# Performance work log

Measured on AMD Instinct MI355X. Metric: run time of the kernel, lower is better.

The kernel has to match this reference:

```python
import jax, jax.numpy as jnp
import numpy as np

BATCH = 256
NUM_PIXELS = 4096
NUM_LATENT = 8192
NUM_STEPS = 50
STEP_SIZE = 0.1
SPARSE_MULT = 0.1
EPS = 1e-8


def setup_inputs() -> dict:
    key = jax.random.key(0)
    k1, k2 = jax.random.split(key)
    input_tensor = jax.random.normal(k1, (BATCH, NUM_PIXELS), dtype=jnp.float32)
    w = jax.random.normal(k2, (NUM_PIXELS, NUM_LATENT), dtype=jnp.float32)
    # l2-normalize each dictionary element (column over pixel dim), as in dp.l2_normalize_weights
    w = w / (jnp.linalg.norm(w, axis=0, keepdims=True) + EPS)
    return {"input_tensor": input_tensor, "w": w}


def _threshold(u):
    # soft threshold with rectify_a=True: a = max(u - lambda, 0)
    return jnp.where(u > SPARSE_MULT, u - SPARSE_MULT, jnp.zeros_like(u))


def reference(input_tensor, w):
    # excitatory drive b = x @ w, constant over inference steps  [B, L]
    excitatory = jnp.matmul(input_tensor, w)
    # inhibitory Gram matrix G = w^T w - I  [L, L]
    gram = jnp.matmul(w.T, w) - jnp.eye(NUM_LATENT, dtype=w.dtype)

    def body(u, _):
        a = _threshold(u)
        du = excitatory - jnp.matmul(a, gram) - u
        return u + STEP_SIZE * du, None

    u0 = jnp.zeros((input_tensor.shape[0], NUM_LATENT), dtype=input_tensor.dtype)
    u_final, _ = jax.lax.scan(body, u0, None, length=NUM_STEPS - 1)
    a_final = _threshold(u_final)
    # reconstruction = a @ w^T  [B, P]
    return jnp.matmul(a_final, w.T)
```

## Files before the change

kernel.cpp:

```cpp
#include <hip/hip_runtime.h>
#include <stdint.h>

#define B_DIM 256
#define P_DIM 4096
#define L_DIM 8192
#define NSTEPS 50
#define STEP 0.1f
#define LAM 0.1f
#define FP8_ITERS 40
#define GSCALE 64.0f
#define ASCALE 16.0f
#define INV_SCALE (1.0f / (64.0f * 16.0f))

typedef __attribute__((ext_vector_type(8))) short bf16x8;
typedef __attribute__((ext_vector_type(4))) float f32x4;
typedef __attribute__((ext_vector_type(2))) long lgx2;

__device__ __forceinline__ unsigned short f2bf(float f) {
    union { float f; uint32_t u; } x; x.f = f;
    uint32_t r = (x.u + 0x7FFF + ((x.u >> 16) & 1)) >> 16;
    return (unsigned short)r;
}
__device__ __forceinline__ float bf2f(unsigned short h) {
    union { uint32_t u; float f; } x; x.u = (uint32_t)h << 16; return x.f;
}


__global__ void cast_x_kernel(const float* __restrict__ in, unsigned short* __restrict__ out, int n) {
    int i = (blockIdx.x * blockDim.x + threadIdx.x) * 4;
    if (i < n) {
        float4 v = *(const float4*)&in[i];
        ushort4 o;
        o.x = f2bf(v.x); o.y = f2bf(v.y); o.z = f2bf(v.z); o.w = f2bf(v.w);
        *(ushort4*)&out[i] = o;
    }
}

__global__ void cast_transpose_w(const float* __restrict__ w,
                                 unsigned short* __restrict__ w_bf,
                                 unsigned short* __restrict__ wT_bf) {
    __shared__ float tile[32][33];
    int c0 = blockIdx.x * 32;
    int r0 = blockIdx.y * 32;
    int tx = threadIdx.x, ty = threadIdx.y;
#pragma unroll
    for (int i = ty; i < 32; i += 8) {
        float v = w[(size_t)(r0 + i) * L_DIM + c0 + tx];
        tile[i][tx] = v;
        w_bf[(size_t)(r0 + i) * L_DIM + c0 + tx] = f2bf(v);
    }
    __syncthreads();
#pragma unroll
    for (int i = ty; i < 32; i += 8) {
        wT_bf[(size_t)(c0 + i) * P_DIM + r0 + tx] = f2bf(tile[tx][i]);
    }
}

__global__ void quantize_G(const unsigned short* __restrict__ G, unsigned char* __restrict__ Gf) {
    size_t i = ((size_t)blockIdx.x * 256 + threadIdx.x) * 8;
    bf16x8 v = *(const bf16x8*)&G[i];
    float f[8];
#pragma unroll
    for (int j = 0; j < 8; ++j) f[j] = bf2f((unsigned short)v[j]) * GSCALE;
    int q0 = __builtin_amdgcn_cvt_pk_fp8_f32(f[0], f[1], 0, false);
    q0 = __builtin_amdgcn_cvt_pk_fp8_f32(f[2], f[3], q0, true);
    int q1 = __builtin_amdgcn_cvt_pk_fp8_f32(f[4], f[5], 0, false);
    q1 = __builtin_amdgcn_cvt_pk_fp8_f32(f[6], f[7], q1, true);
    const int r = (int)(i & 127);
    size_t dst = (i & ~(size_t)127) + (size_t)((((r >> 6) & 1) << 6) + (((r >> 3) & 3) << 4) + (((r >> 5) & 1) << 3));
    *(int2*)(Gf + dst) = make_int2(q0, q1);
}

template <int BM, int BN, int BK, int WMC, int WNC, int EPI, int MM, int NN, int KK, int MAP>
__global__ __launch_bounds__(WMC * WNC * 64)
void gemm_pipe(const unsigned short* __restrict__ A,
               const unsigned short* __restrict__ Bt,
               float* __restrict__ Cf,
               float* __restrict__ uvec,
               unsigned short* __restrict__ aout,
               unsigned char* __restrict__ afp8) {
    constexpr int NWAVES = WMC * WNC;
    constexpr int WM = BM / WMC, WN = BN / WNC;
    constexpr int MF = WM / 16, NF = WN / 16;
    constexpr int ACH = BM / (8 * NWAVES);
    constexpr int BCH = BN / (8 * NWAVES);
    constexpr int LPS = ACH + BCH;
    constexpr int NT = KK / BK;
    static_assert(BK == 64, "swizzle hardcoded for BK=64");
    static_assert(ACH * 8 * NWAVES == BM && BCH * 8 * NWAVES == BN, "stage geometry");
    static_assert(NT % 4 == 0 && NT >= 8, "pipeline geometry");

    __shared__ __align__(16) unsigned short As[4][BM * BK];
    __shared__ __align__(16) unsigned short Bs[4][BN * BK];

    const int tid = threadIdx.x;
    const int w = tid >> 6;
    const int l = tid & 63;
    const int wr = w / WNC, wc = w % WNC;

    const int id = blockIdx.x;
    int bx, by;
    if constexpr (MAP == 0) {
        constexpr int PPX = (NN / BN) / 8;
        static_assert(MM / BM == 4 && (NN / BN) % 8 == 0, "panel map geometry");
        bx = (id & 7) * PPX + ((id >> 3) >> 2);
        by = (id >> 3) & 3;
    } else {
        constexpr int GY = MM / BM;
        by = id % GY;
        bx = id / GY;
    }
    const int row0 = by * BM;
    const int col0 = bx * BN;

    const int lrow = l >> 3;
    const int lcol = (((l & 7) ^ lrow) * 8);

    const unsigned short* gA = A + (size_t)(row0 + lrow) * KK + lcol;
    const unsigned short* gB = Bt + (size_t)(col0 + lrow) * KK + lcol;

    auto stage = [&](int buf, int k0) {
#pragma unroll
        for (int i = 0; i < ACH; ++i) {
            const int chunk = i * NWAVES + w;
            __builtin_amdgcn_global_load_lds(
                (const __attribute__((address_space(1))) void*)(gA + (size_t)chunk * 8 * KK + k0),
                (__attribute__((address_space(3))) void*)(&As[buf][chunk * 512]), 16, 0, 0);
        }
#pragma unroll
        for (int i = 0; i < BCH; ++i) {
            const int chunk = i * NWAVES + w;
            __builtin_amdgcn_global_load_lds(
                (const __attribute__((address_space(1))) void*)(gB + (size_t)chunk * 8 * KK + k0),
                (__attribute__((address_space(3))) void*)(&Bs[buf][chunk * 512]), 16, 0, 0);
        }
    };

    f32x4 acc[MF][NF] = {};

    auto compute = [&](int buf) {
#pragma unroll
        for (int kk = 0; kk < BK; kk += 32) {
            const int kslot = (kk >> 3) + (l >> 4);
            bf16x8 af[MF], bfr[NF];
#pragma unroll
            for (int mf = 0; mf < MF; ++mf) {
                const int arow = wr * WM + mf * 16 + (l & 15);
                af[mf] = *(const bf16x8*)&As[buf][arow * BK + ((kslot ^ (arow & 7)) << 3)];
            }
#pragma unroll
            for (int nf = 0; nf < NF; ++nf) {
                const int brow = wc * WN + nf * 16 + (l & 15);
                bfr[nf] = *(const bf16x8*)&Bs[buf][brow * BK + ((kslot ^ (brow & 7)) << 3)];
            }
#pragma unroll
            for (int mf = 0; mf < MF; ++mf)
#pragma unroll
                for (int nf = 0; nf < NF; ++nf)
                    acc[mf][nf] = __builtin_amdgcn_mfma_f32_16x16x32_bf16(
                        af[mf], bfr[nf], acc[mf][nf], 0, 0, 0);
        }
    };

#define PH(BUF, TT, WAITN, DOSTG)                                            \
    asm volatile("s_waitcnt vmcnt(%0)" ::"i"(WAITN) : "memory");             \
    __builtin_amdgcn_s_barrier();                                            \
    asm volatile("" ::: "memory");                                           \
    if (DOSTG) stage((BUF + 3) & 3, ((TT) + 3) * BK);                        \
    compute(BUF);

    stage(0, 0);
    stage(1, BK);
    stage(2, 2 * BK);
#pragma unroll 1
    for (int t = 0; t < NT - 4; t += 4) {
        PH(0, t + 0, 2 * LPS, true)
        PH(1, t + 1, 2 * LPS, true)
        PH(2, t + 2, 2 * LPS, true)
        PH(3, t + 3, 2 * LPS, true)
    }
    PH(0, NT - 4, 2 * LPS, true)
    PH(1, NT - 3, 2 * LPS, false)
    PH(2, NT - 2, LPS, false)
    PH(3, NT - 1, 0, false)
#undef PH

    const int er = (l >> 4) * 4;
    const int ec = l & 15;
#pragma unroll
    for (int mf = 0; mf < MF; ++mf) {
#pragma unroll
        for (int nf = 0; nf < NF; ++nf) {
#pragma unroll
            for (int j = 0; j < 4; ++j) {
                int gr = row0 + wr * WM + mf * 16 + er + j;
                int gc = col0 + wc * WN + nf * 16 + ec;
                size_t idx = (size_t)gr * NN + gc;
                float v = acc[mf][nf][j];
                if constexpr (EPI == 1) {
                    Cf[idx] = v;
                    float u0 = STEP * v;
                    uvec[idx] = u0;
                    float a = (u0 > LAM) ? (u0 - LAM) : 0.0f;
                    aout[idx] = f2bf(a);
                    float a16 = a * ASCALE;
                    int q = __builtin_amdgcn_cvt_pk_fp8_f32(a16, a16, 0, false);
                    const int r = gc & 127;
                    size_t fd = (size_t)gr * L_DIM + (size_t)(gc & ~127) +
                                (size_t)((((r >> 6) & 1) << 6) + (((r >> 3) & 3) << 4) + (((r >> 5) & 1) << 3) + (r & 7));
                    afp8[fd] = (unsigned char)(q & 0xff);
                } else {
                    Cf[idx] = v;
                }
            }
        }
    }
}

template <int BM, int BN, int WMC, int WNC, int EPI, int KROW, int KLOOP, int MAP>
__global__ __launch_bounds__(WMC * WNC * 64, 2)
void gemm2(const unsigned short* __restrict__ A,
           const unsigned short* __restrict__ Bt,
           unsigned short* __restrict__ Obf) {
    constexpr int NWAVES = WMC * WNC;
    constexpr int WM = BM / WMC, WN = BN / WNC;
    constexpr int MF = WM / 16, NF = WN / 16;
    constexpr int ACH = BM / (8 * NWAVES);
    constexpr int BCH = BN / (8 * NWAVES);
    constexpr int LPS = ACH + BCH;
    constexpr int BK = 64;
    constexpr int NT = KLOOP / BK;
    static_assert(ACH * 8 * NWAVES == BM && BCH * 8 * NWAVES == BN, "stage geometry");
    static_assert(NT % 2 == 0 && NT >= 4, "pipeline geometry");

    __shared__ __align__(16) unsigned short As[2][BM * BK];
    __shared__ __align__(16) unsigned short Bs[2][BN * BK];

    const int tid = threadIdx.x;
    const int w = tid >> 6;
    const int l = tid & 63;
    const int wr = w / WNC, wc = w % WNC;

    const int id = blockIdx.x;
    int bx, by, koff;
    size_t o_off;
    if constexpr (MAP == 2) {
        const int sb = id >> 4, wi = id & 15;
        by = (sb >> 3) * 4 + (wi >> 2);
        bx = (sb & 7) * 4 + (wi & 3);
        koff = 0;
        o_off = 0;
    } else {
        const int xcd = id & 7;
        by = (id >> 3) & 1;
        const int pp = id >> 4;
        const int slice = pp & 3;
        bx = xcd * 4 + (pp >> 2);
        koff = slice * KLOOP;
        o_off = (size_t)slice * B_DIM * L_DIM;
    }
    const int row0 = by * BM;
    const int col0 = bx * BN;

    const int lrow = l >> 3;
    const int lcol = (((l & 7) ^ lrow) * 8);

    const unsigned short* gA = A + (size_t)(row0 + lrow) * KROW + koff + lcol;
    const unsigned short* gB = Bt + (size_t)(col0 + lrow) * KROW + koff + lcol;

    auto stage = [&](int buf, int t) {
        const int k0 = t * BK;
#pragma unroll
        for (int i = 0; i < ACH; ++i) {
            const int chunk = i * NWAVES + w;
            __builtin_amdgcn_global_load_lds(
                (const __attribute__((address_space(1))) void*)(gA + (size_t)chunk * 8 * KROW + k0),
                (__attribute__((address_space(3))) void*)(&As[buf][chunk * 512]), 16, 0, 0);
        }
#pragma unroll
        for (int i = 0; i < BCH; ++i) {
            const int chunk = i * NWAVES + w;
            __builtin_amdgcn_global_load_lds(
                (const __attribute__((address_space(1))) void*)(gB + (size_t)chunk * 8 * KROW + k0),
                (__attribute__((address_space(3))) void*)(&Bs[buf][chunk * 512]), 16, 0, 0);
        }
    };

    f32x4 acc[MF][NF] = {};

    auto compute = [&](int buf) {
#pragma unroll
        for (int kk = 0; kk < BK; kk += 32) {
            const int kslot = (kk >> 3) + (l >> 4);
            bf16x8 af[MF], bfr[NF];
#pragma unroll
            for (int mf = 0; mf < MF; ++mf) {
                const int arow = wr * WM + mf * 16 + (l & 15);
                af[mf] = *(const bf16x8*)&As[buf][arow * BK + ((kslot ^ (arow & 7)) << 3)];
            }
#pragma unroll
            for (int nf = 0; nf < NF; ++nf) {
                const int brow = wc * WN + nf * 16 + (l & 15);
                bfr[nf] = *(const bf16x8*)&Bs[buf][brow * BK + ((kslot ^ (brow & 7)) << 3)];
            }
#pragma unroll
            for (int mf = 0; mf < MF; ++mf)
#pragma unroll
                for (int nf = 0; nf < NF; ++nf)
                    acc[mf][nf] = __builtin_amdgcn_mfma_f32_16x16x32_bf16(
                        af[mf], bfr[nf], acc[mf][nf], 0, 0, 0);
        }
    };

#define PH2(BUF, WAITN, DOSTG, TT)                                           \
    asm volatile("s_waitcnt vmcnt(%0)" ::"i"(WAITN) : "memory");             \
    __builtin_amdgcn_s_barrier();                                            \
    asm volatile("" ::: "memory");                                           \
    compute(BUF);                                                            \
    __builtin_amdgcn_s_barrier();                                            \
    asm volatile("" ::: "memory");                                           \
    if (DOSTG) stage(BUF, (TT) + 2);

    stage(0, 0);
    stage(1, 1);
#pragma unroll 1
    for (int t = 0; t < NT - 2; t += 2) {
        PH2(0, LPS, true, t)
        PH2(1, LPS, true, t + 1)
    }
    PH2(0, LPS, false, 0)
    PH2(1, 0, false, 0)
#undef PH2

    const int er = (l >> 4) * 4;
    const int ec = l & 15;
#pragma unroll
    for (int mf = 0; mf < MF; ++mf) {
#pragma unroll
        for (int nf = 0; nf < NF; ++nf) {
#pragma unroll
            for (int j = 0; j < 4; ++j) {
                int gr = row0 + wr * WM + mf * 16 + er + j;
                int gc = col0 + wc * WN + nf * 16 + ec;
                float v = acc[mf][nf][j];
                if constexpr (EPI == 0) {
                    if (gr == gc) v -= 1.0f;
                    Obf[(size_t)gr * L_DIM + gc] = f2bf(v);
                } else {
                    Obf[o_off + (size_t)gr * L_DIM + gc] = f2bf(v);
                }
            }
        }
    }
}

template <int BM, int BN, int WMC, int WNC>
__global__ __launch_bounds__(WMC * WNC * 64, 2)
void gemm_fp8(const unsigned char* __restrict__ A,
              const unsigned char* __restrict__ Bt,
              unsigned short* __restrict__ Obf) {
    constexpr int NWAVES = WMC * WNC;
    constexpr int WM = BM / WMC, WN = BN / WNC;
    constexpr int MF = WM / 16, NF = WN / 16;
    constexpr int BKB = 128;
    constexpr int ACH = BM / (8 * NWAVES);
    constexpr int BCH = BN / (8 * NWAVES);
    constexpr int LPS = ACH + BCH;
    constexpr int KLOOP = 2048;
    constexpr int NT = KLOOP / BKB;
    constexpr int KKB = L_DIM;
    static_assert(ACH * 8 * NWAVES == BM && BCH * 8 * NWAVES == BN, "stage geometry");

    __shared__ __align__(16) unsigned char As[2][BM * BKB];
    __shared__ __align__(16) unsigned char Bs[2][BN * BKB];

    const int tid = threadIdx.x;
    const int w = tid >> 6;
    const int l = tid & 63;
    const int wr = w / WNC, wc = w % WNC;

    const int id = blockIdx.x;
    const int xcd = id & 7;
    const int by = (id >> 3) & 1;
    const int pp = id >> 4;
    const int slice = pp & 3;
    const int bx = xcd * 4 + (pp >> 2);
    const int row0 = by * BM;
    const int col0 = bx * BN;
    const int koff = slice * KLOOP;

    const int lrow = l >> 3;
    const int lcol = (((l & 7) ^ lrow) << 4);

    const unsigned char* gA = A + (size_t)(row0 + lrow) * KKB + koff + lcol;
    const unsigned char* gB = Bt + (size_t)(col0 + lrow) * KKB + koff + lcol;

    auto stage = [&](int buf, int t) {
        const int k0 = t * BKB;
#pragma unroll
        for (int i = 0; i < ACH; ++i) {
            const int chunk = i * NWAVES + w;
            __builtin_amdgcn_global_load_lds(
                (const __attribute__((address_space(1))) void*)(gA + (size_t)chunk * 8 * KKB + k0),
                (__attribute__((address_space(3))) void*)(&As[buf][chunk * 1024]), 16, 0, 0);
        }
#pragma unroll
        for (int i = 0; i < BCH; ++i) {
            const int chunk = i * NWAVES + w;
            __builtin_amdgcn_global_load_lds(
                (const __attribute__((address_space(1))) void*)(gB + (size_t)chunk * 8 * KKB + k0),
                (__attribute__((address_space(3))) void*)(&Bs[buf][chunk * 1024]), 16, 0, 0);
        }
    };

    f32x4 acc[MF][NF] = {};

    auto compute = [&](int buf) {
#pragma unroll
        for (int kp = 0; kp < 2; ++kp) {
            const int c = kp * 4 + (l >> 4);
            lgx2 af[MF], bfr[NF];
#pragma unroll
            for (int mf = 0; mf < MF; ++mf) {
                const int arow = wr * WM + mf * 16 + (l & 15);
                af[mf] = *(const lgx2*)&As[buf][arow * BKB + ((c ^ (arow & 7)) << 4)];
            }
#pragma unroll
            for (int nf = 0; nf < NF; ++nf) {
                const int brow = wc * WN + nf * 16 + (l & 15);
                bfr[nf] = *(const lgx2*)&Bs[buf][brow * BKB + ((c ^ (brow & 7)) << 4)];
            }
#pragma unroll
            for (int mf = 0; mf < MF; ++mf)
#pragma unroll
                for (int nf = 0; nf < NF; ++nf) {
                    acc[mf][nf] = __builtin_amdgcn_mfma_f32_16x16x32_fp8_fp8(
                        af[mf][0], bfr[nf][0], acc[mf][nf], 0, 0, 0);
                    acc[mf][nf] = __builtin_amdgcn_mfma_f32_16x16x32_fp8_fp8(
                        af[mf][1], bfr[nf][1], acc[mf][nf], 0, 0, 0);
                }
        }
    };

#define PH2(BUF, WAITN, DOSTG, TT)                                           \
    asm volatile("s_waitcnt vmcnt(%0)" ::"i"(WAITN) : "memory");             \
    __builtin_amdgcn_s_barrier();                                            \
    asm volatile("" ::: "memory");                                           \
    compute(BUF);                                                            \
    __builtin_amdgcn_s_barrier();                                            \
    asm volatile("" ::: "memory");                                           \
    if (DOSTG) stage(BUF, (TT) + 2);

    stage(0, 0);
    stage(1, 1);
#pragma unroll 1
    for (int t = 0; t < NT - 2; t += 2) {
        PH2(0, LPS, true, t)
        PH2(1, LPS, true, t + 1)
    }
    PH2(0, LPS, false, 0)
    PH2(1, 0, false, 0)
#undef PH2

    const int er = (l >> 4) * 4;
    const int ec = l & 15;
    const size_t o_off = (size_t)slice * B_DIM * L_DIM;
#pragma unroll
    for (int mf = 0; mf < MF; ++mf)
#pragma unroll
        for (int nf = 0; nf < NF; ++nf)
#pragma unroll
            for (int j = 0; j < 4; ++j) {
                int gr = row0 + wr * WM + mf * 16 + er + j;
                int gc = col0 + wc * WN + nf * 16 + ec;
                Obf[o_off + (size_t)gr * L_DIM + gc] = f2bf(acc[mf][nf][j] * INV_SCALE);
            }
}

__global__ void reduce_iter(const unsigned short* __restrict__ P,
                            const float* __restrict__ bv,
                            float* __restrict__ uv,
                            unsigned short* __restrict__ an,
                            unsigned char* __restrict__ anf) {
    constexpr size_t SL = (size_t)B_DIM * L_DIM;
    size_t i = ((size_t)blockIdx.x * 256 + threadIdx.x) * 8;
    float s[8] = {};
#pragma unroll
    for (int sl = 0; sl < 4; ++sl) {
        ushort4 p0 = *(const ushort4*)&P[sl * SL + i];
        ushort4 p1 = *(const ushort4*)&P[sl * SL + i + 4];
        s[0] += bf2f(p0.x); s[1] += bf2f(p0.y); s[2] += bf2f(p0.z); s[3] += bf2f(p0.w);
        s[4] += bf2f(p1.x); s[5] += bf2f(p1.y); s[6] += bf2f(p1.z); s[7] += bf2f(p1.w);
    }
    float4 b0 = *(const float4*)&bv[i];
    float4 b1 = *(const float4*)&bv[i + 4];
    float4 u0 = *(const float4*)&uv[i];
    float4 u1 = *(const float4*)&uv[i + 4];
    float un[8];
    un[0] = 0.9f * u0.x + STEP * b0.x - STEP * s[0];
    un[1] = 0.9f * u0.y + STEP * b0.y - STEP * s[1];
    un[2] = 0.9f * u0.z + STEP * b0.z - STEP * s[2];
    un[3] = 0.9f * u0.w + STEP * b0.w - STEP * s[3];
    un[4] = 0.9f * u1.x + STEP * b1.x - STEP * s[4];
    un[5] = 0.9f * u1.y + STEP * b1.y - STEP * s[5];
    un[6] = 0.9f * u1.z + STEP * b1.z - STEP * s[6];
    un[7] = 0.9f * u1.w + STEP * b1.w - STEP * s[7];
    *(float4*)&uv[i] = make_float4(un[0], un[1], un[2], un[3]);
    *(float4*)&uv[i + 4] = make_float4(un[4], un[5], un[6], un[7]);
    float a[8];
#pragma unroll
    for (int j = 0; j < 8; ++j) a[j] = (un[j] > LAM) ? (un[j] - LAM) : 0.0f;
    ushort4 o0, o1;
    o0.x = f2bf(a[0]); o0.y = f2bf(a[1]); o0.z = f2bf(a[2]); o0.w = f2bf(a[3]);
    o1.x = f2bf(a[4]); o1.y = f2bf(a[5]); o1.z = f2bf(a[6]); o1.w = f2bf(a[7]);
    *(ushort4*)&an[i] = o0;
    *(ushort4*)&an[i + 4] = o1;
    int q0 = __builtin_amdgcn_cvt_pk_fp8_f32(a[0] * ASCALE, a[1] * ASCALE, 0, false);
    q0 = __builtin_amdgcn_cvt_pk_fp8_f32(a[2] * ASCALE, a[3] * ASCALE, q0, true);
    int q1 = __builtin_amdgcn_cvt_pk_fp8_f32(a[4] * ASCALE, a[5] * ASCALE, 0, false);
    q1 = __builtin_amdgcn_cvt_pk_fp8_f32(a[6] * ASCALE, a[7] * ASCALE, q1, true);
    const int r = (int)(i & 127);
    size_t dst = (i & ~(size_t)127) + (size_t)((((r >> 6) & 1) << 6) + (((r >> 3) & 3) << 4) + (((r >> 5) & 1) << 3));
    *(int2*)(anf + dst) = make_int2(q0, q1);
}

extern "C" void kernel_launch(void* const* d_in, const int* in_sizes, int n_in,
                              void* d_out, int out_size, void* d_ws, size_t ws_size,
                              hipStream_t stream) {
    (void)in_sizes; (void)n_in; (void)out_size; (void)ws_size;
    const float* x = (const float*)d_in[0];
    const float* w = (const float*)d_in[1];
    float* out = (float*)d_out;

    char* ws = (char*)d_ws;
    unsigned short* wT  = (unsigned short*)ws;
    unsigned char*  Gf  = (unsigned char*)ws;
    unsigned short* wbf = wT + (size_t)L_DIM * P_DIM;
    unsigned short* G   = wbf + (size_t)P_DIM * L_DIM;
    float* bv = (float*)(G + (size_t)L_DIM * L_DIM);
    float* uv = bv + (size_t)B_DIM * L_DIM;
    unsigned short* a0 = (unsigned short*)(uv + (size_t)B_DIM * L_DIM);
    unsigned short* a1 = a0 + (size_t)B_DIM * L_DIM;
    unsigned short* xbf = a1 + (size_t)B_DIM * L_DIM;
    unsigned char* a0f = (unsigned char*)(xbf + (size_t)B_DIM * P_DIM);
    unsigned char* a1f = a0f + (size_t)B_DIM * L_DIM;
    unsigned short* Ppart = (unsigned short*)(a1f + (size_t)B_DIM * L_DIM);

    cast_x_kernel<<<(B_DIM * P_DIM / 4 + 255) / 256, 256, 0, stream>>>(x, xbf, B_DIM * P_DIM);
    cast_transpose_w<<<dim3(L_DIM / 32, P_DIM / 32), dim3(32, 8), 0, stream>>>(w, wbf, wT);

    gemm2<256, 256, 2, 4, 0, P_DIM, P_DIM, 2><<<1024, 512, 0, stream>>>(wT, wT, G);

    gemm_pipe<64, 128, 64, 2, 4, 1, B_DIM, L_DIM, P_DIM, 0><<<256, 512, 0, stream>>>(
        xbf, wT, bv, uv, a0, a0f);

    quantize_G<<<(int)(((size_t)L_DIM * L_DIM / 8) / 256), 256, 0, stream>>>(G, Gf);

    unsigned short* ac = a0; unsigned short* an = a1;
    unsigned char* acf = a0f; unsigned char* anf = a1f;
    for (int it = 0; it < FP8_ITERS; ++it) {
        gemm_fp8<128, 256, 2, 4><<<256, 512, 0, stream>>>(acf, Gf, Ppart);
        reduce_iter<<<(B_DIM * L_DIM) / (256 * 8), 256, 0, stream>>>(Ppart, bv, uv, an, anf);
        unsigned short* t = ac; ac = an; an = t;
        unsigned char* tf = acf; acf = anf; anf = tf;
    }
    for (int it = 0; it < (NSTEPS - 2) - FP8_ITERS; ++it) {
        gemm2<128, 256, 2, 4, 4, L_DIM, 2048, 3><<<256, 512, 0, stream>>>(ac, G, Ppart);
        reduce_iter<<<(B_DIM * L_DIM) / (256 * 8), 256, 0, stream>>>(Ppart, bv, uv, an, anf);
        unsigned short* t = ac; ac = an; an = t;
        unsigned char* tf = acf; acf = anf; anf = tf;
    }

    gemm_pipe<64, 64, 64, 2, 4, 3, B_DIM, P_DIM, L_DIM, 0><<<256, 512, 0, stream>>>(
        ac, wbf, out, nullptr, nullptr, nullptr);
}
```

Before: 2.298 ms.

## Compute Gram matrix from upper-triangular tiles and mirror via transpose

Replaces the full 1024-block Gram GEMM with a symmetric kernel that computes only the 528 upper-triangular 256x256 tiles, mapped from a linear block id by closed-form triangular indexing. Off-diagonal tiles are transposed through LDS and written to the mirrored location. This roughly halves the MFMA work for the w^T w precompute, at the cost of extra transposed stores, a float-sqrt index mapping, and a partial second wave of blocks.

```diff
diff --git a/kernel.cpp b/kernel.cpp
--- a/kernel.cpp
+++ b/kernel.cpp
@@ -1,5 +1,6 @@
 #include <hip/hip_runtime.h>
 #include <stdint.h>
+#include <math.h>
 
 #define B_DIM 256
 #define P_DIM 4096
@@ -217,6 +218,150 @@
     }
 }
 
+__global__ __launch_bounds__(512, 2)
+void gemm_gram_sym(const unsigned short* __restrict__ A,
+                   unsigned short* __restrict__ G) {
+    constexpr int BM = 256, BN = 256, BK = 64;
+    constexpr int WMC = 2, WNC = 4, NWAVES = 8;
+    constexpr int WM = 128, WN = 64, MF = 8, NF = 4;
+    constexpr int ACH = 4, BCH = 4, LPS = 8;
+    constexpr int NT = P_DIM / BK;
+
+    __shared__ __align__(16) unsigned short sh[4 * 256 * 64];
+#define ASB(buf) (sh + (buf) * (256 * 64))
+#define BSB(buf) (sh + (2 + (buf)) * (256 * 64))
+
+    const int tid = threadIdx.x;
+    const int w = tid >> 6;
+    const int l = tid & 63;
+    const int wr = w / WNC, wc = w % WNC;
+
+    const int id = blockIdx.x;
+    const int i = (int)((65.0f - sqrtf(4225.0f - 8.0f * (float)id)) * 0.5f);
+    const int cum = i * (65 - i) / 2;
+    const int j = i + (id - cum);
+    const int by = i, bx = j;
+    const int row0 = by * BM;
+    const int col0 = bx * BN;
+
+    const int lrow = l >> 3;
+    const int lcol = (((l & 7) ^ lrow) * 8);
+
+    const unsigned short* gA = A + (size_t)(row0 + lrow) * P_DIM + lcol;
+    const unsigned short* gB = A + (size_t)(col0 + lrow) * P_DIM + lcol;
+
+    auto stage = [&](int buf, int t) {
+        const int k0 = t * BK;
+#pragma unroll
+        for (int c = 0; c < ACH; ++c) {
+            const int chunk = c * NWAVES + w;
+            __builtin_amdgcn_global_load_lds(
+                (const __attribute__((address_space(1))) void*)(gA + (size_t)chunk * 8 * P_DIM + k0),
+                (__attribute__((address_space(3))) void*)(ASB(buf) + chunk * 512), 16, 0, 0);
+        }
+#pragma unroll
+        for (int c = 0; c < BCH; ++c) {
+            const int chunk = c * NWAVES + w;
+            __builtin_amdgcn_global_load_lds(
+                (const __attribute__((address_space(1))) void*)(gB + (size_t)chunk * 8 * P_DIM + k0),
+                (__attribute__((address_space(3))) void*)(BSB(buf) + chunk * 512), 16, 0, 0);
+        }
+    };
+
+    f32x4 acc[MF][NF] = {};
+
+    auto compute = [&](int buf) {
+#pragma unroll
+        for (int kk = 0; kk < BK; kk += 32) {
+            const int kslot = (kk >> 3) + (l >> 4);
+            bf16x8 af[MF], bfr[NF];
+#pragma unroll
+            for (int mf = 0; mf < MF; ++mf) {
+                const int arow = wr * WM + mf * 16 + (l & 15);
+                af[mf] = *(const bf16x8*)&ASB(buf)[arow * BK + ((kslot ^ (arow & 7)) << 3)];
+            }
+#pragma unroll
+            for (int nf = 0; nf < NF; ++nf) {
+                const int brow = wc * WN + nf * 16 + (l & 15);
+                bfr[nf] = *(const bf16x8*)&BSB(buf)[brow * BK + ((kslot ^ (brow & 7)) << 3)];
+            }
+#pragma unroll
+            for (int mf = 0; mf < MF; ++mf)
+#pragma unroll
+                for (int nf = 0; nf < NF; ++nf)
+                    acc[mf][nf] = __builtin_amdgcn_mfma_f32_16x16x32_bf16(
+                        af[mf], bfr[nf], acc[mf][nf], 0, 0, 0);
+        }
+    };
+
+#define PH2(BUF, WAITN, DOSTG, TT)                                           \
+    asm volatile("s_waitcnt vmcnt(%0)" ::"i"(WAITN) : "memory");             \
+    __builtin_amdgcn_s_barrier();                                            \
+    asm volatile("" ::: "memory");                                           \
+    compute(BUF);                                                            \
+    __builtin_amdgcn_s_barrier();                                            \
+    asm volatile("" ::: "memory");                                           \
+    if (DOSTG) stage(BUF, (TT) + 2);
+
+    stage(0, 0);
+    stage(1, 1);
+#pragma unroll 1
+    for (int t = 0; t < NT - 2; t += 2) {
+        PH2(0, LPS, true, t)
+        PH2(1, LPS, true, t + 1)
+    }
+    PH2(0, LPS, false, 0)
+    PH2(1, 0, false, 0)
+#undef PH2
+
+    const int er = (l >> 4) * 4;
+    const int ec = l & 15;
+
+#pragma unroll
+    for (int mf = 0; mf < MF; ++mf)
+#pragma unroll
+        for (int nf = 0; nf < NF; ++nf)
+#pragma unroll
+            for (int jj = 0; jj < 4; ++jj) {
+                int gr = row0 + wr * WM + mf * 16 + er + jj;
+                int gc = col0 + wc * WN + nf * 16 + ec;
+                float v = acc[mf][nf][jj];
+                if (gr == gc) v -= 1.0f;
+                G[(size_t)gr * L_DIM + gc] = f2bf(v);
+            }
+
+    if (by != bx) {
+        unsigned short* T = sh;
+#pragma unroll 1
+        for (int p = 0; p < 2; ++p) {
+            __syncthreads();
+            if ((wc >> 1) == p) {
+#pragma unroll
+                for (int mf = 0; mf < MF; ++mf)
+#pragma unroll
+                    for (int nf = 0; nf < NF; ++nf)
+#pragma unroll
+                        for (int jj = 0; jj < 4; ++jj) {
+                            const int gr_l = wr * WM + mf * 16 + er + jj;
+                            const int gc_l = (wc & 1) * 64 + nf * 16 + ec;
+                            T[gc_l * 256 + (gr_l ^ ((gc_l & 7) << 2))] = f2bf(acc[mf][nf][jj]);
+                        }
+            }
+            __syncthreads();
+            const int rr = tid >> 6;
+            const int cc = (tid & 63) * 4;
+#pragma unroll
+            for (int s = 0; s < 16; ++s) {
+                const int r = s * 8 + rr;
+                uint2 val = *(const uint2*)&T[r * 256 + (cc ^ ((r & 7) << 2))];
+                *(uint2*)&G[(size_t)(col0 + p * 128 + r) * L_DIM + row0 + cc] = val;
+            }
+        }
+    }
+#undef ASB
+#undef BSB
+}
+
 template <int BM, int BN, int WMC, int WNC, int EPI, int KROW, int KLOOP, int MAP>
 __global__ __launch_bounds__(WMC * WNC * 64, 2)
 void gemm2(const unsigned short* __restrict__ A,
@@ -549,7 +694,7 @@
     cast_x_kernel<<<(B_DIM * P_DIM / 4 + 255) / 256, 256, 0, stream>>>(x, xbf, B_DIM * P_DIM);
     cast_transpose_w<<<dim3(L_DIM / 32, P_DIM / 32), dim3(32, 8), 0, stream>>>(w, wbf, wT);
 
-    gemm2<256, 256, 2, 4, 0, P_DIM, P_DIM, 2><<<1024, 512, 0, stream>>>(wT, wT, G);
+    gemm_gram_sym<<<528, 512, 0, stream>>>(wT, G);
 
     gemm_pipe<64, 128, 64, 2, 4, 1, B_DIM, L_DIM, P_DIM, 0><<<256, 512, 0, stream>>>(
         xbf, wT, bv, uv, a0, a0f);
```

New measurement: 2.199 ms. 1.05x faster.
